# Kernel tuning notes

Hardware: AMD Instinct MI355X
Metric: run time of the kernel (lower is better)

The kernel has to match this reference:

```python
import jax, jax.numpy as jnp
import numpy as np

B, T, C, H, N = 2, 1024, 1024, 16, 64
D_DECAY, D_AAA, D_MV, D_GATE = 64, 64, 32, 128
LN_EPS = 64e-5  # GroupNorm eps used by RWKV7 (1e-5 * head_size_divisor**2)


def setup_inputs():
    key = jax.random.key(0)
    ks = jax.random.split(key, 32)
    rn = lambda k, shape, s=1.0: jax.random.normal(k, shape, jnp.float32) * s
    p = {}
    p['x'] = rn(ks[0], (B, T, C))
    p['v_first'] = rn(ks[1], (B, T, C))
    for i, nm in enumerate(['x_r', 'x_w', 'x_k', 'x_v', 'x_a', 'x_g']):
        p[nm] = jax.random.uniform(ks[2 + i], (1, 1, C), jnp.float32)
    p['w1'] = rn(ks[8], (C, D_DECAY), 0.02); p['w2'] = rn(ks[9], (D_DECAY, C), 0.02); p['w0'] = rn(ks[10], (C,), 0.5)
    p['a1'] = rn(ks[11], (C, D_AAA), 0.02); p['a2'] = rn(ks[12], (D_AAA, C), 0.02); p['a0'] = rn(ks[13], (C,), 0.1)
    p['v1'] = rn(ks[14], (C, D_MV), 0.02); p['v2'] = rn(ks[15], (D_MV, C), 0.02); p['v0'] = rn(ks[16], (C,), 0.1)
    p['g1'] = rn(ks[17], (C, D_GATE), 0.02); p['g2'] = rn(ks[18], (D_GATE, C), 0.02)
    p['k_k'] = jax.random.uniform(ks[19], (1, 1, C), jnp.float32)
    p['k_a'] = jax.random.uniform(ks[20], (1, 1, C), jnp.float32)
    p['r_k'] = rn(ks[21], (H, N), 0.1)
    s = C ** -0.5
    p['W_r'] = rn(ks[22], (C, C), s); p['W_k'] = rn(ks[23], (C, C), s)
    p['W_v'] = rn(ks[24], (C, C), s); p['W_o'] = rn(ks[25], (C, C), s)
    p['ln_w'] = jnp.ones((C,), jnp.float32); p['ln_b'] = jnp.zeros((C,), jnp.float32)
    return p


def _rwkv7_op(r, w, k, v, a, b):
    # r,w,k,v,a,b: (B,T,C). Per-head matrix-state recurrence:
    #   S_t = S_{t-1} * diag(decay_t) + (S_{t-1} @ a_t) b_t^T + v_t k_t^T ; out_t = S_t @ r_t
    f = lambda z: z.reshape(B, T, H, N).astype(jnp.float32).transpose(1, 0, 2, 3)  # (T,B,H,N)
    r_, k_, v_, a_, b_ = f(r), f(k), f(v), f(a), f(b)
    d_ = jnp.exp(-jnp.exp(f(w)))  # decay in (0,1)

    def step(S, inp):
        rt, dt, kt, vt, at, bt = inp  # each (B,H,N)
        sa = jnp.einsum('bhij,bhj->bhi', S, at)
        S = S * dt[:, :, None, :] + sa[..., None] * bt[:, :, None, :] + vt[..., None] * kt[:, :, None, :]
        return S, jnp.einsum('bhij,bhj->bhi', S, rt)

    S0 = jnp.zeros((B, H, N, N), jnp.float32)
    _, out = jax.lax.scan(step, S0, (r_, d_, k_, v_, a_, b_))
    return out.transpose(1, 0, 2, 3).reshape(B, T, C)


def _forward(x, v_first, x_r, x_w, x_k, x_v, x_a, x_g, w1, w2, w0, a1, a2, a0,
             v1, v2, v0, g1, g2, k_k, k_a, r_k, W_r, W_k, W_v, W_o, ln_w, ln_b):
    xx = jnp.pad(x, ((0, 0), (1, 0), (0, 0)))[:, :T] - x  # token shift
    xr = x + xx * x_r; xw = x + xx * x_w; xk = x + xx * x_k
    xv = x + xx * x_v; xa = x + xx * x_a; xg = x + xx * x_g
    r = xr @ W_r
    w = -jax.nn.softplus(-(jnp.tanh(xw @ w1) @ w2 + w0)) - 0.5
    k = xk @ W_k
    v = xv @ W_v
    v = v + (v_first - v) * jax.nn.sigmoid(xv @ v1 @ v2 + v0)  # layer_id > 0 branch
    a = jax.nn.sigmoid(xa @ a1 @ a2 + a0)
    g = jax.nn.sigmoid(xg @ g1) @ g2
    kk = (k * k_k).reshape(B, T, H, N)
    kk = (kk / jnp.maximum(jnp.linalg.norm(kk, axis=-1, keepdims=True), 1e-12)).reshape(B, T, C)
    k = k * (1.0 + (a - 1.0) * k_a)
    y = _rwkv7_op(r, w, k, v, -kk, kk * a)
    # GroupNorm(H groups over C) applied per token
    yh = y.reshape(B, T, H, N)
    mu = yh.mean(-1, keepdims=True)
    var = yh.var(-1, keepdims=True)
    y = ((yh - mu) / jnp.sqrt(var + LN_EPS)).reshape(B, T, C) * ln_w + ln_b
    rh = r.reshape(B, T, H, N); kh = k.reshape(B, T, H, N); vh = v.reshape(B, T, H, N)
    y = y + ((rh * kh * r_k).sum(-1, keepdims=True) * vh).reshape(B, T, C)
    return (y * g) @ W_o


def reference(x, v_first, x_r, x_w, x_k, x_v, x_a, x_g, w1, w2, w0, a1, a2, a0,
              v1, v2, v0, g1, g2, k_k, k_a, r_k, W_r, W_k, W_v, W_o, ln_w, ln_b):
    out = _forward(x, v_first, x_r, x_w, x_k, x_v, x_a, x_g, w1, w2, w0, a1, a2, a0,
                   v1, v2, v0, g1, g2, k_k, k_a, r_k, W_r, W_k, W_v, W_o, ln_w, ln_b)
    return (out, v_first)
```

## Files before the change

kernel.cpp:

```cpp
#include <hip/hip_runtime.h>
#include <hip/hip_bf16.h>
#include <cstdint>
#include <cstddef>

typedef __hip_bfloat16 bf16;
typedef __bf16 bf16x8 __attribute__((ext_vector_type(8)));
typedef float f32x4 __attribute__((ext_vector_type(4)));

#define BB 2
#define TT 1024
#define CC 1024
#define HH 16
#define PKS 448
#define PKB 1792
#define CH 8
#define NCH 4
#define STEPB 2048
#define CHB (CH * STEPB)
#define NC (TT / CH)

__device__ __forceinline__ bf16 f2b(float v){ return __float2bfloat16(v); }

__device__ __forceinline__ float hex_add(float x) {
    x += __int_as_float(__builtin_amdgcn_mov_dpp(__float_as_int(x), 0xB1, 0xF, 0xF, true));
    x += __int_as_float(__builtin_amdgcn_mov_dpp(__float_as_int(x), 0x4E, 0xF, 0xF, true));
    x += __int_as_float(__builtin_amdgcn_mov_dpp(__float_as_int(x), 0x141, 0xF, 0xF, true));
    x += __int_as_float(__builtin_amdgcn_mov_dpp(__float_as_int(x), 0x140, 0xF, 0xF, true));
    return x;
}

typedef __attribute__((address_space(3))) void as3_void;
typedef __attribute__((address_space(1))) const void as1_void;
__device__ __forceinline__ void gload_lds16(const void* g, void* l) {
    __builtin_amdgcn_global_load_lds((as1_void*)g, (as3_void*)l, 16, 0, 0);
}

struct TrDesc { const float* in; bf16* out; int R, S; };
struct TrArgs { TrDesc d[12]; };

__global__ __launch_bounds__(256) void transpose_batch(TrArgs args)
{
    TrDesc t = args.d[blockIdx.z];
    __shared__ float tile[32][33];
    int s0 = blockIdx.x * 32, r0 = blockIdx.y * 32;
    if (s0 >= t.S || r0 >= t.R) return;
    int tx = threadIdx.x & 31, ty = threadIdx.x >> 5;
#pragma unroll
    for (int i = 0; i < 4; i++) {
        int r = r0 + ty + i * 8, s = s0 + tx;
        if (r < t.R && s < t.S) tile[ty + i * 8][tx] = t.in[(size_t)r * t.S + s];
    }
    __syncthreads();
#pragma unroll
    for (int i = 0; i < 4; i++) {
        int s = s0 + ty + i * 8, r = r0 + tx;
        if (s < t.S && r < t.R) t.out[(size_t)s * t.R + r] = f2b(tile[tx][ty + i * 8]);
    }
}

__global__ __launch_bounds__(256) void mix_kernel(
    const float* __restrict__ x, const float* __restrict__ vfirst,
    const float* __restrict__ mr, const float* __restrict__ mw, const float* __restrict__ mk,
    const float* __restrict__ mv, const float* __restrict__ ma, const float* __restrict__ mg,
    bf16* __restrict__ xr, bf16* __restrict__ xw, bf16* __restrict__ xk,
    bf16* __restrict__ xv, bf16* __restrict__ xa, bf16* __restrict__ xg,
    float* __restrict__ vout)
{
    int row = blockIdx.x;
    int t = row & (TT - 1);
    size_t base = (size_t)row * CC;
    for (int c = threadIdx.x; c < CC; c += 256) {
        float xc = x[base + c];
        float xp = (t > 0) ? x[base - CC + c] : 0.f;
        float d = xp - xc;
        xr[base + c] = f2b(xc + d * mr[c]);
        xw[base + c] = f2b(xc + d * mw[c]);
        xk[base + c] = f2b(xc + d * mk[c]);
        xv[base + c] = f2b(xc + d * mv[c]);
        xa[base + c] = f2b(xc + d * ma[c]);
        xg[base + c] = f2b(xc + d * mg[c]);
        vout[base + c] = vfirst[base + c];
    }
}

template <class EmitF>
__device__ __forceinline__ void gemm_tile(const bf16* __restrict__ A, const bf16* __restrict__ BT,
                                          int K, int m0, int n0, EmitF emit)
{
    __shared__ __align__(16) bf16 Atile[128 * 32];
    __shared__ __align__(16) bf16 Btile[128 * 32];
    int tid = threadIdx.x;
    int w = tid >> 6, lane = tid & 63;
    int wr = w >> 1, wc = w & 1;
    int quad = lane >> 4, l16 = lane & 15;

    f32x4 zero = {0.f, 0.f, 0.f, 0.f};
    f32x4 acc[4][4];
#pragma unroll
    for (int i = 0; i < 4; i++)
#pragma unroll
        for (int j = 0; j < 4; j++) acc[i][j] = zero;

    int rr = lane >> 2;
    int cs = lane & 3;
    int ra0 = w * 32 + rr;
    int ra1 = ra0 + 16;
    int cg0 = cs ^ ((ra0 >> 1) & 3);
    int cg1 = cs ^ ((ra1 >> 1) & 3);

    for (int k0 = 0; k0 < K; k0 += 32) {
        uint4 av0 = *reinterpret_cast<const uint4*>(A  + (size_t)(m0 + ra0) * K + k0 + cg0 * 8);
        uint4 av1 = *reinterpret_cast<const uint4*>(A  + (size_t)(m0 + ra1) * K + k0 + cg1 * 8);
        uint4 bv0 = *reinterpret_cast<const uint4*>(BT + (size_t)(n0 + ra0) * K + k0 + cg0 * 8);
        uint4 bv1 = *reinterpret_cast<const uint4*>(BT + (size_t)(n0 + ra1) * K + k0 + cg1 * 8);
        __syncthreads();
        *reinterpret_cast<uint4*>(&Atile[ra0 * 32 + cs * 8]) = av0;
        *reinterpret_cast<uint4*>(&Atile[ra1 * 32 + cs * 8]) = av1;
        *reinterpret_cast<uint4*>(&Btile[ra0 * 32 + cs * 8]) = bv0;
        *reinterpret_cast<uint4*>(&Btile[ra1 * 32 + cs * 8]) = bv1;
        __syncthreads();

        bf16x8 af[4], bfr[4];
#pragma unroll
        for (int mi = 0; mi < 4; mi++) {
            int m = wr * 64 + mi * 16 + l16;
            int c2 = quad ^ ((m >> 1) & 3);
            af[mi] = *reinterpret_cast<const bf16x8*>(&Atile[m * 32 + c2 * 8]);
        }
#pragma unroll
        for (int ni = 0; ni < 4; ni++) {
            int n = wc * 64 + ni * 16 + l16;
            int c2 = quad ^ ((n >> 1) & 3);
            bfr[ni] = *reinterpret_cast<const bf16x8*>(&Btile[n * 32 + c2 * 8]);
        }
#pragma unroll
        for (int mi = 0; mi < 4; mi++)
#pragma unroll
            for (int ni = 0; ni < 4; ni++)
                acc[mi][ni] = __builtin_amdgcn_mfma_f32_16x16x32_bf16(af[mi], bfr[ni], acc[mi][ni], 0, 0, 0);
    }

#pragma unroll
    for (int mi = 0; mi < 4; mi++)
#pragma unroll
        for (int ni = 0; ni < 4; ni++)
#pragma unroll
            for (int rg = 0; rg < 4; rg++) {
                int m = m0 + wr * 64 + mi * 16 + quad * 4 + rg;
                int n = n0 + wc * 64 + ni * 16 + l16;
                emit(m, n, acc[mi][ni][rg]);
            }
}

struct B3Args { const bf16* A[3]; const bf16* BT[3]; float* out[3]; };
__global__ __launch_bounds__(256) void big3_kernel(B3Args args)
{
    int z = blockIdx.z;
    float* out = args.out[z];
    gemm_tile(args.A[z], args.BT[z], 1024, blockIdx.x * 128, blockIdx.y * 128,
              [&](int m, int n, float v) { out[(size_t)m * 1024 + n] = v; });
}

struct L1Desc { const bf16* A; const bf16* BT; bf16* outB; int N; int mode; };
struct L1Args { L1Desc d[4]; };
__global__ __launch_bounds__(256) void lora1_kernel(L1Args args)
{
    L1Desc dz = args.d[blockIdx.z];
    gemm_tile(dz.A, dz.BT, 1024, blockIdx.x * 128, 0,
              [&](int m, int n, float v) {
                  if (n < dz.N) {
                      float r = (dz.mode == 2) ? tanhf(v)
                              : (dz.mode == 3) ? 1.f / (1.f + expf(-v)) : v;
                      dz.outB[(size_t)m * dz.N + n] = f2b(r);
                  }
              });
}

struct L2Desc { const bf16* A; const bf16* BT; const float* bias; float* outF; int K; int mode; };
struct L2Args { L2Desc d[4]; const float* vraw; const float* vfirst; };
__global__ __launch_bounds__(256) void lora2_kernel(L2Args args)
{
    L2Desc dz = args.d[blockIdx.z];
    gemm_tile(dz.A, dz.BT, dz.K, blockIdx.x * 128, blockIdx.y * 128,
              [&](int m, int n, float v) {
                  size_t idx = (size_t)m * 1024 + n;
                  if (dz.mode == 4) {
                      float xx = v + dz.bias[n];
                      float ww = -log1pf(expf(-xx)) - 0.5f;
                      dz.outF[idx] = expf(-expf(ww));
                  } else if (dz.mode == 5) {
                      float xx = v + dz.bias[n];
                      dz.outF[idx] = 1.f / (1.f + expf(-xx));
                  } else if (dz.mode == 6) {
                      float gate = 1.f / (1.f + expf(-(v + dz.bias[n])));
                      float vr = args.vraw[idx];
                      dz.outF[idx] = vr + (args.vfirst[idx] - vr) * gate;
                  } else {
                      dz.outF[idx] = v;
                  }
              });
}

__global__ __launch_bounds__(256) void final_kernel(const bf16* __restrict__ A, const bf16* __restrict__ BT,
                                                    float* __restrict__ out)
{
    gemm_tile(A, BT, 1024, blockIdx.x * 128, blockIdx.y * 128,
              [&](int m, int n, float v) { out[(size_t)m * 1024 + n] = v; });
}

__global__ __launch_bounds__(256) void pack_kernel(
    float* __restrict__ k, const float* __restrict__ a, const float* __restrict__ r,
    const float* __restrict__ v, const float* __restrict__ dw,
    const float* __restrict__ kkw, const float* __restrict__ kaw,
    float* __restrict__ PK)
{
    int tid = threadIdx.x;
    int wave = tid >> 6, lane = tid & 63;
    int idx = blockIdx.x * 4 + wave;
    size_t off = (size_t)idx * 64 + lane;
    int c = (idx & 15) * 64 + lane;
    float kraw = k[off];
    float av = a[off];
    float kkv = kraw * kkw[c];
    float s = kkv * kkv;
#pragma unroll
    for (int m = 32; m; m >>= 1) s += __shfl_xor(s, m);
    float kkn = kkv / fmaxf(sqrtf(s), 1e-12f);
    float ks = kraw * (1.f + (av - 1.f) * kaw[c]);
    k[off] = ks;
    float bb = kkn * av;
    float rv = r[off];
    float dv = dw[off];
    float bt = bb * rv, ct = ks * rv;
#pragma unroll
    for (int m = 32; m; m >>= 1) { bt += __shfl_xor(bt, m); ct += __shfl_xor(ct, m); }
    int b = idx >> 14;
    int h = idx & 15;
    int t = (idx >> 4) & (TT - 1);
    size_t sidx = (size_t)(b * HH + h) * TT + t;
    float* pw = PK + sidx * PKS;
    pw[lane] = ks; pw[64 + lane] = kkn; pw[128 + lane] = bb; pw[192 + lane] = v[off];
    pw[256 + lane] = rv; pw[320 + lane] = dv;
    if (lane == 0) { pw[384] = bt; pw[385] = ct; }
}

struct SetR { f32x4 q, d, r, k, b; float vi; float2 bc; };

__device__ __forceinline__ void ds_load_set(SetR& s, const char* slot, int c16, int row)
{
    s.q  = *(const f32x4*)(slot + 256  + c16);
    s.d  = *(const f32x4*)(slot + 1280 + c16);
    s.r  = *(const f32x4*)(slot + 1024 + c16);
    s.k  = *(const f32x4*)(slot + 0    + c16);
    s.b  = *(const f32x4*)(slot + 512  + c16);
    s.vi = *(const float*)(slot + 768 + row * 4);
    s.bc = *(const float2*)(slot + 1536);
}

__device__ __forceinline__ float step4(const SetR& sd, f32x4& S)
{
    f32x4 Sd   = S * sd.d;
    f32x4 sacv = S * sd.q;
    f32x4 oacv = Sd * sd.r;
    float sar = (sacv[0] + sacv[1]) + (sacv[2] + sacv[3]);
    float od  = (oacv[0] + oacv[1]) + (oacv[2] + oacv[3]);
    sar = hex_add(sar);
    od  = hex_add(od);
    float sa = -sar;
    float o = fmaf(sd.vi, sd.bc.y, fmaf(sa, sd.bc.x, od));
    S = Sd + sa * sd.b + sd.vi * sd.k;
    return o;
}

__global__ __launch_bounds__(256, 1) void scan_kernel(
    const float* __restrict__ PK, float* __restrict__ ybuf)
{
    __shared__ __align__(16) char ring[NCH * CHB];
    const int tid = threadIdx.x;
    const int wid = tid >> 6, lane = tid & 63;
    const int xcd = blockIdx.x & 7, kk = blockIdx.x >> 3;
    const int bh = xcd * 4 + (kk >> 4);
    const int wq = kk & 15;
    const int b = bh >> 4, h = bh & 15;
    const int row = wq * 4 + (lane >> 4);
    const int c = lane & 15;
    const int c16 = c * 16;

    const char* base = (const char*)(PK + (size_t)bh * TT * PKS);
    const char* g1 = base + lane * 16;
    const char* g2 = g1 + 1024;

    auto stage_chunk = [&](int ci) {
        const char* p1 = g1 + (size_t)ci * CH * PKB;
        const char* p2 = g2 + (size_t)ci * CH * PKB;
        char* s = ring + (ci & (NCH - 1)) * CHB;
        for (int j = wid - 1; j < CH; j += 3) {
            gload_lds16(p1 + (size_t)j * PKB, s + j * STEPB);
            gload_lds16(p2 + (size_t)j * PKB, s + j * STEPB + 1024);
        }
    };

    if (wid > 0) {
        stage_chunk(0);
        stage_chunk(1);
        stage_chunk(2);
        asm volatile("s_waitcnt vmcnt(0)" ::: "memory");
    }
    __builtin_amdgcn_sched_barrier(0);
    __builtin_amdgcn_s_barrier();
    __builtin_amdgcn_sched_barrier(0);

    f32x4 S = {0.f, 0.f, 0.f, 0.f};
    SetR X, Y;
    if (wid == 0) ds_load_set(X, ring, c16, row);
    float* py = ybuf + (size_t)b * TT * CC + h * 64 + row;

    for (int i = 0; i < NC; i++) {
        if (wid == 0) {
            const char* sl  = ring + (i & (NCH - 1)) * CHB;
            const char* sln = ring + ((i + 1) & (NCH - 1)) * CHB;
            float o;
            ds_load_set(Y, sl + 1 * STEPB, c16, row); o = step4(X, S); if (c == 0) *py = o; py += CC;
            ds_load_set(X, sl + 2 * STEPB, c16, row); o = step4(Y, S); if (c == 0) *py = o; py += CC;
            ds_load_set(Y, sl + 3 * STEPB, c16, row); o = step4(X, S); if (c == 0) *py = o; py += CC;
            ds_load_set(X, sl + 4 * STEPB, c16, row); o = step4(Y, S); if (c == 0) *py = o; py += CC;
            ds_load_set(Y, sl + 5 * STEPB, c16, row); o = step4(X, S); if (c == 0) *py = o; py += CC;
            ds_load_set(X, sl + 6 * STEPB, c16, row); o = step4(Y, S); if (c == 0) *py = o; py += CC;
            ds_load_set(Y, sl + 7 * STEPB, c16, row); o = step4(X, S); if (c == 0) *py = o; py += CC;
            ds_load_set(X, sln,            c16, row); o = step4(Y, S); if (c == 0) *py = o; py += CC;
        } else {
            if (i + 3 < NC) {
                stage_chunk(i + 3);
                if (wid == 3) asm volatile("s_waitcnt vmcnt(4)" ::: "memory");
                else          asm volatile("s_waitcnt vmcnt(6)" ::: "memory");
            } else {
                asm volatile("s_waitcnt vmcnt(0)" ::: "memory");
            }
        }
        __builtin_amdgcn_sched_barrier(0);
        __builtin_amdgcn_s_barrier();
        __builtin_amdgcn_sched_barrier(0);
    }
}

__global__ __launch_bounds__(256) void gn_kernel(
    const float* __restrict__ y, const float* __restrict__ r, const float* __restrict__ k,
    const float* __restrict__ v, const float* __restrict__ g,
    const float* __restrict__ lnw, const float* __restrict__ lnb,
    const float* __restrict__ rk, bf16* __restrict__ z)
{
    int tid = threadIdx.x;
    int idx = blockIdx.x * 4 + (tid >> 6);
    int lane = tid & 63;
    size_t off = (size_t)idx * 64 + lane;
    int c = (idx & 15) * 64 + lane;
    float yv = y[off];
    float rv = r[off], kv = k[off], vv = v[off];
    float s1 = yv, s2 = yv * yv, s3 = rv * kv * rk[c];
#pragma unroll
    for (int m = 32; m; m >>= 1) {
        s1 += __shfl_xor(s1, m);
        s2 += __shfl_xor(s2, m);
        s3 += __shfl_xor(s3, m);
    }
    float mu = s1 * (1.f / 64.f);
    float var = fmaxf(s2 * (1.f / 64.f) - mu * mu, 0.f);
    float yn = (yv - mu) * rsqrtf(var + 64e-5f) * lnw[c] + lnb[c];
    float out = (yn + s3 * vv) * g[off];
    z[off] = f2b(out);
}

extern "C" void kernel_launch(void* const* d_in, const int* in_sizes, int n_in,
                              void* d_out, int out_size, void* d_ws, size_t ws_size,
                              hipStream_t stream)
{
    const float* x       = (const float*)d_in[0];
    const float* v_first = (const float*)d_in[1];
    const float* x_r = (const float*)d_in[2];
    const float* x_w = (const float*)d_in[3];
    const float* x_k = (const float*)d_in[4];
    const float* x_v = (const float*)d_in[5];
    const float* x_a = (const float*)d_in[6];
    const float* x_g = (const float*)d_in[7];
    const float* w1 = (const float*)d_in[8];
    const float* w2 = (const float*)d_in[9];
    const float* w0 = (const float*)d_in[10];
    const float* a1 = (const float*)d_in[11];
    const float* a2 = (const float*)d_in[12];
    const float* a0 = (const float*)d_in[13];
    const float* v1 = (const float*)d_in[14];
    const float* v2 = (const float*)d_in[15];
    const float* v0 = (const float*)d_in[16];
    const float* g1 = (const float*)d_in[17];
    const float* g2 = (const float*)d_in[18];
    const float* k_k = (const float*)d_in[19];
    const float* k_a = (const float*)d_in[20];
    const float* r_k = (const float*)d_in[21];
    const float* W_r = (const float*)d_in[22];
    const float* W_k = (const float*)d_in[23];
    const float* W_v = (const float*)d_in[24];
    const float* W_o = (const float*)d_in[25];
    const float* ln_w = (const float*)d_in[26];
    const float* ln_b = (const float*)d_in[27];

    const size_t BTC = (size_t)BB * TT * CC;
    const int M = BB * TT;

    char* ws = (char*)d_ws;
    size_t off = 0;
    auto alloc = [&](size_t bytes) -> char* {
        char* p = ws + off;
        off += (bytes + 255) & ~(size_t)255;
        return p;
    };

    bf16* xr = (bf16*)alloc(BTC * 2);
    bf16* xw = (bf16*)alloc(BTC * 2);
    bf16* xk = (bf16*)alloc(BTC * 2);
    bf16* xv = (bf16*)alloc(BTC * 2);
    bf16* xa = (bf16*)alloc(BTC * 2);
    bf16* xg = (bf16*)alloc(BTC * 2);
    bf16* WrT = (bf16*)alloc(1024 * 1024 * 2);
    bf16* WkT = (bf16*)alloc(1024 * 1024 * 2);
    bf16* WvT = (bf16*)alloc(1024 * 1024 * 2);
    bf16* w1T = (bf16*)alloc(128 * 1024 * 2);
    bf16* a1T = (bf16*)alloc(128 * 1024 * 2);
    bf16* v1T = (bf16*)alloc(128 * 1024 * 2);
    bf16* g1T = (bf16*)alloc(128 * 1024 * 2);
    bf16* w2T = (bf16*)alloc(1024 * 64 * 2);
    bf16* a2T = (bf16*)alloc(1024 * 64 * 2);
    bf16* v2T = (bf16*)alloc(1024 * 32 * 2);
    bf16* g2T = (bf16*)alloc(1024 * 128 * 2);
    bf16* h_w = (bf16*)alloc((size_t)M * 64 * 2);
    bf16* h_a = (bf16*)alloc((size_t)M * 64 * 2);
    bf16* h_v = (bf16*)alloc((size_t)M * 32 * 2);
    bf16* h_g = (bf16*)alloc((size_t)M * 128 * 2);

    float* PK = (float*)ws;
    size_t pk_end = (size_t)BB * HH * TT * PKS * 4;
    if (off < pk_end) off = pk_end;
    off = (off + 255) & ~(size_t)255;

    bf16* WoT = (bf16*)alloc(1024 * 1024 * 2);
    float* rbuf = (float*)alloc(BTC * 4);
    float* kbuf = (float*)alloc(BTC * 4);
    float* vraw = (float*)alloc(BTC * 4);
    float* vbuf = (float*)alloc(BTC * 4);
    float* dbuf = (float*)alloc(BTC * 4);
    float* abuf = (float*)alloc(BTC * 4);
    float* gbuf = (float*)alloc(BTC * 4);

    float* ybuf = vraw;
    bf16*  zbuf = (bf16*)dbuf;

    (void)in_sizes; (void)n_in; (void)out_size; (void)ws_size;

    TrArgs ta;
    ta.d[0]  = {W_r, WrT, 1024, 1024};
    ta.d[1]  = {W_k, WkT, 1024, 1024};
    ta.d[2]  = {W_v, WvT, 1024, 1024};
    ta.d[3]  = {W_o, WoT, 1024, 1024};
    ta.d[4]  = {w1, w1T, 1024, 64};
    ta.d[5]  = {a1, a1T, 1024, 64};
    ta.d[6]  = {v1, v1T, 1024, 32};
    ta.d[7]  = {g1, g1T, 1024, 128};
    ta.d[8]  = {w2, w2T, 64, 1024};
    ta.d[9]  = {a2, a2T, 64, 1024};
    ta.d[10] = {v2, v2T, 32, 1024};
    ta.d[11] = {g2, g2T, 128, 1024};
    transpose_batch<<<dim3(32, 32, 12), 256, 0, stream>>>(ta);

    float* vout = (float*)d_out + BTC;
    mix_kernel<<<BB * TT, 256, 0, stream>>>(x, v_first, x_r, x_w, x_k, x_v, x_a, x_g,
                                            xr, xw, xk, xv, xa, xg, vout);

    B3Args b3;
    b3.A[0] = xr; b3.A[1] = xk; b3.A[2] = xv;
    b3.BT[0] = WrT; b3.BT[1] = WkT; b3.BT[2] = WvT;
    b3.out[0] = rbuf; b3.out[1] = kbuf; b3.out[2] = vraw;
    big3_kernel<<<dim3(16, 8, 3), 256, 0, stream>>>(b3);

    L1Args l1;
    l1.d[0] = {xw, w1T, h_w, 64, 2};
    l1.d[1] = {xa, a1T, h_a, 64, 0};
    l1.d[2] = {xv, v1T, h_v, 32, 0};
    l1.d[3] = {xg, g1T, h_g, 128, 3};
    lora1_kernel<<<dim3(16, 1, 4), 256, 0, stream>>>(l1);

    L2Args l2;
    l2.d[0] = {h_w, w2T, w0, dbuf, 64, 4};
    l2.d[1] = {h_a, a2T, a0, abuf, 64, 5};
    l2.d[2] = {h_v, v2T, v0, vbuf, 32, 6};
    l2.d[3] = {h_g, g2T, nullptr, gbuf, 128, 0};
    l2.vraw = vraw; l2.vfirst = v_first;
    lora2_kernel<<<dim3(16, 8, 4), 256, 0, stream>>>(l2);

    pack_kernel<<<BB * TT * HH / 4, 256, 0, stream>>>(kbuf, abuf, rbuf, vbuf, dbuf, k_k, k_a, PK);

    scan_kernel<<<BB * HH * 16, 256, 0, stream>>>(PK, ybuf);

    gn_kernel<<<BB * TT * HH / 4, 256, 0, stream>>>(ybuf, rbuf, kbuf, vbuf, gbuf, ln_w, ln_b, r_k, zbuf);

    final_kernel<<<dim3(16, 8), 256, 0, stream>>>(zbuf, WoT, (float*)d_out);
}
```

Measured before the change: 426.3 us.

## Merge prep launches, fuse projection and LoRA-down GEMMs, use direct global-to-LDS loads

The weight-transpose and token-mix kernels become one launch, with the mix work placed in an extra z-slice. The three big projections and the four LoRA-down GEMMs now share a single launch, and LoRA blocks with y>0 exit early. The GEMM tile loader now uses global_load_lds so data goes straight from global memory into LDS without passing through registers. The aim is to cut launch overhead and tail gaps and to lower register pressure during staging. The LDS layout from direct loads must match the swizzled reads the old explicit stores produced, which is a correctness risk.

```diff
diff --git a/kernel.cpp b/kernel.cpp
--- a/kernel.cpp
+++ b/kernel.cpp
@@ -36,50 +36,53 @@
 }
 
 struct TrDesc { const float* in; bf16* out; int R, S; };
-struct TrArgs { TrDesc d[12]; };
-
-__global__ __launch_bounds__(256) void transpose_batch(TrArgs args)
-{
-    TrDesc t = args.d[blockIdx.z];
-    __shared__ float tile[32][33];
-    int s0 = blockIdx.x * 32, r0 = blockIdx.y * 32;
-    if (s0 >= t.S || r0 >= t.R) return;
-    int tx = threadIdx.x & 31, ty = threadIdx.x >> 5;
-#pragma unroll
-    for (int i = 0; i < 4; i++) {
-        int r = r0 + ty + i * 8, s = s0 + tx;
-        if (r < t.R && s < t.S) tile[ty + i * 8][tx] = t.in[(size_t)r * t.S + s];
-    }
-    __syncthreads();
-#pragma unroll
-    for (int i = 0; i < 4; i++) {
-        int s = s0 + ty + i * 8, r = r0 + tx;
-        if (s < t.S && r < t.R) t.out[(size_t)s * t.R + r] = f2b(tile[tx][ty + i * 8]);
-    }
-}
-
-__global__ __launch_bounds__(256) void mix_kernel(
-    const float* __restrict__ x, const float* __restrict__ vfirst,
-    const float* __restrict__ mr, const float* __restrict__ mw, const float* __restrict__ mk,
-    const float* __restrict__ mv, const float* __restrict__ ma, const float* __restrict__ mg,
-    bf16* __restrict__ xr, bf16* __restrict__ xw, bf16* __restrict__ xk,
-    bf16* __restrict__ xv, bf16* __restrict__ xa, bf16* __restrict__ xg,
-    float* __restrict__ vout)
-{
-    int row = blockIdx.x;
-    int t = row & (TT - 1);
-    size_t base = (size_t)row * CC;
-    for (int c = threadIdx.x; c < CC; c += 256) {
-        float xc = x[base + c];
-        float xp = (t > 0) ? x[base - CC + c] : 0.f;
-        float d = xp - xc;
-        xr[base + c] = f2b(xc + d * mr[c]);
-        xw[base + c] = f2b(xc + d * mw[c]);
-        xk[base + c] = f2b(xc + d * mk[c]);
-        xv[base + c] = f2b(xc + d * mv[c]);
-        xa[base + c] = f2b(xc + d * ma[c]);
-        xg[base + c] = f2b(xc + d * mg[c]);
-        vout[base + c] = vfirst[base + c];
+struct PrepArgs {
+    TrDesc d[12];
+    const float* x; const float* vfirst;
+    const float *mr, *mw, *mk, *mv, *ma, *mg;
+    bf16 *xr, *xw, *xk, *xv, *xa, *xg;
+    float* vout;
+};
+
+__global__ __launch_bounds__(256) void prep_kernel(PrepArgs args)
+{
+    if (blockIdx.z < 12) {
+        TrDesc t = args.d[blockIdx.z];
+        __shared__ float tile[32][33];
+        int s0 = blockIdx.x * 32, r0 = blockIdx.y * 32;
+        if (s0 >= t.S || r0 >= t.R) return;
+        int tx = threadIdx.x & 31, ty = threadIdx.x >> 5;
+#pragma unroll
+        for (int i = 0; i < 4; i++) {
+            int r = r0 + ty + i * 8, s = s0 + tx;
+            if (r < t.R && s < t.S) tile[ty + i * 8][tx] = t.in[(size_t)r * t.S + s];
+        }
+        __syncthreads();
+#pragma unroll
+        for (int i = 0; i < 4; i++) {
+            int s = s0 + ty + i * 8, r = r0 + tx;
+            if (s < t.S && r < t.R) t.out[(size_t)s * t.R + r] = f2b(tile[tx][ty + i * 8]);
+        }
+        return;
+    }
+    int bid = blockIdx.y * 32 + blockIdx.x;
+#pragma unroll
+    for (int rr = 0; rr < 2; rr++) {
+        int row = bid * 2 + rr;
+        int t = row & (TT - 1);
+        size_t base = (size_t)row * CC;
+        for (int c = threadIdx.x; c < CC; c += 256) {
+            float xc = args.x[base + c];
+            float xp = (t > 0) ? args.x[base - CC + c] : 0.f;
+            float d = xp - xc;
+            args.xr[base + c] = f2b(xc + d * args.mr[c]);
+            args.xw[base + c] = f2b(xc + d * args.mw[c]);
+            args.xk[base + c] = f2b(xc + d * args.mk[c]);
+            args.xv[base + c] = f2b(xc + d * args.mv[c]);
+            args.xa[base + c] = f2b(xc + d * args.ma[c]);
+            args.xg[base + c] = f2b(xc + d * args.mg[c]);
+            args.vout[base + c] = args.vfirst[base + c];
+        }
     }
 }
 
@@ -108,16 +111,15 @@
     int cg0 = cs ^ ((ra0 >> 1) & 3);
     int cg1 = cs ^ ((ra1 >> 1) & 3);
 
+    bf16* atb = Atile + w * 1024;
+    bf16* btb = Btile + w * 1024;
+
     for (int k0 = 0; k0 < K; k0 += 32) {
-        uint4 av0 = *reinterpret_cast<const uint4*>(A  + (size_t)(m0 + ra0) * K + k0 + cg0 * 8);
-        uint4 av1 = *reinterpret_cast<const uint4*>(A  + (size_t)(m0 + ra1) * K + k0 + cg1 * 8);
-        uint4 bv0 = *reinterpret_cast<const uint4*>(BT + (size_t)(n0 + ra0) * K + k0 + cg0 * 8);
-        uint4 bv1 = *reinterpret_cast<const uint4*>(BT + (size_t)(n0 + ra1) * K + k0 + cg1 * 8);
         __syncthreads();
-        *reinterpret_cast<uint4*>(&Atile[ra0 * 32 + cs * 8]) = av0;
-        *reinterpret_cast<uint4*>(&Atile[ra1 * 32 + cs * 8]) = av1;
-        *reinterpret_cast<uint4*>(&Btile[ra0 * 32 + cs * 8]) = bv0;
-        *reinterpret_cast<uint4*>(&Btile[ra1 * 32 + cs * 8]) = bv1;
+        gload_lds16(A  + (size_t)(m0 + ra0) * K + k0 + cg0 * 8, atb);
+        gload_lds16(A  + (size_t)(m0 + ra1) * K + k0 + cg1 * 8, atb + 512);
+        gload_lds16(BT + (size_t)(n0 + ra0) * K + k0 + cg0 * 8, btb);
+        gload_lds16(BT + (size_t)(n0 + ra1) * K + k0 + cg1 * 8, btb + 512);
         __syncthreads();
 
         bf16x8 af[4], bfr[4];
@@ -152,20 +154,20 @@
             }
 }
 
-struct B3Args { const bf16* A[3]; const bf16* BT[3]; float* out[3]; };
-__global__ __launch_bounds__(256) void big3_kernel(B3Args args)
+struct L1Desc { const bf16* A; const bf16* BT; bf16* outB; int N; int mode; };
+struct ProjArgs { const bf16* A[3]; const bf16* BT[3]; float* out[3]; L1Desc d[4]; };
+
+__global__ __launch_bounds__(256) void proj_kernel(ProjArgs args)
 {
     int z = blockIdx.z;
-    float* out = args.out[z];
-    gemm_tile(args.A[z], args.BT[z], 1024, blockIdx.x * 128, blockIdx.y * 128,
-              [&](int m, int n, float v) { out[(size_t)m * 1024 + n] = v; });
-}
-
-struct L1Desc { const bf16* A; const bf16* BT; bf16* outB; int N; int mode; };
-struct L1Args { L1Desc d[4]; };
-__global__ __launch_bounds__(256) void lora1_kernel(L1Args args)
-{
-    L1Desc dz = args.d[blockIdx.z];
+    if (z < 3) {
+        float* out = args.out[z];
+        gemm_tile(args.A[z], args.BT[z], 1024, blockIdx.x * 128, blockIdx.y * 128,
+                  [&](int m, int n, float v) { out[(size_t)m * 1024 + n] = v; });
+        return;
+    }
+    if (blockIdx.y) return;
+    L1Desc dz = args.d[z - 3];
     gemm_tile(dz.A, dz.BT, 1024, blockIdx.x * 128, 0,
               [&](int m, int n, float v) {
                   if (n < dz.N) {
@@ -455,37 +457,34 @@
 
     (void)in_sizes; (void)n_in; (void)out_size; (void)ws_size;
 
-    TrArgs ta;
-    ta.d[0]  = {W_r, WrT, 1024, 1024};
-    ta.d[1]  = {W_k, WkT, 1024, 1024};
-    ta.d[2]  = {W_v, WvT, 1024, 1024};
-    ta.d[3]  = {W_o, WoT, 1024, 1024};
-    ta.d[4]  = {w1, w1T, 1024, 64};
-    ta.d[5]  = {a1, a1T, 1024, 64};
-    ta.d[6]  = {v1, v1T, 1024, 32};
-    ta.d[7]  = {g1, g1T, 1024, 128};
-    ta.d[8]  = {w2, w2T, 64, 1024};
-    ta.d[9]  = {a2, a2T, 64, 1024};
-    ta.d[10] = {v2, v2T, 32, 1024};
-    ta.d[11] = {g2, g2T, 128, 1024};
-    transpose_batch<<<dim3(32, 32, 12), 256, 0, stream>>>(ta);
-
-    float* vout = (float*)d_out + BTC;
-    mix_kernel<<<BB * TT, 256, 0, stream>>>(x, v_first, x_r, x_w, x_k, x_v, x_a, x_g,
-                                            xr, xw, xk, xv, xa, xg, vout);
-
-    B3Args b3;
-    b3.A[0] = xr; b3.A[1] = xk; b3.A[2] = xv;
-    b3.BT[0] = WrT; b3.BT[1] = WkT; b3.BT[2] = WvT;
-    b3.out[0] = rbuf; b3.out[1] = kbuf; b3.out[2] = vraw;
-    big3_kernel<<<dim3(16, 8, 3), 256, 0, stream>>>(b3);
-
-    L1Args l1;
-    l1.d[0] = {xw, w1T, h_w, 64, 2};
-    l1.d[1] = {xa, a1T, h_a, 64, 0};
-    l1.d[2] = {xv, v1T, h_v, 32, 0};
-    l1.d[3] = {xg, g1T, h_g, 128, 3};
-    lora1_kernel<<<dim3(16, 1, 4), 256, 0, stream>>>(l1);
+    PrepArgs pa;
+    pa.d[0]  = {W_r, WrT, 1024, 1024};
+    pa.d[1]  = {W_k, WkT, 1024, 1024};
+    pa.d[2]  = {W_v, WvT, 1024, 1024};
+    pa.d[3]  = {W_o, WoT, 1024, 1024};
+    pa.d[4]  = {w1, w1T, 1024, 64};
+    pa.d[5]  = {a1, a1T, 1024, 64};
+    pa.d[6]  = {v1, v1T, 1024, 32};
+    pa.d[7]  = {g1, g1T, 1024, 128};
+    pa.d[8]  = {w2, w2T, 64, 1024};
+    pa.d[9]  = {a2, a2T, 64, 1024};
+    pa.d[10] = {v2, v2T, 32, 1024};
+    pa.d[11] = {g2, g2T, 128, 1024};
+    pa.x = x; pa.vfirst = v_first;
+    pa.mr = x_r; pa.mw = x_w; pa.mk = x_k; pa.mv = x_v; pa.ma = x_a; pa.mg = x_g;
+    pa.xr = xr; pa.xw = xw; pa.xk = xk; pa.xv = xv; pa.xa = xa; pa.xg = xg;
+    pa.vout = (float*)d_out + BTC;
+    prep_kernel<<<dim3(32, 32, 13), 256, 0, stream>>>(pa);
+
+    ProjArgs pj;
+    pj.A[0] = xr; pj.A[1] = xk; pj.A[2] = xv;
+    pj.BT[0] = WrT; pj.BT[1] = WkT; pj.BT[2] = WvT;
+    pj.out[0] = rbuf; pj.out[1] = kbuf; pj.out[2] = vraw;
+    pj.d[0] = {xw, w1T, h_w, 64, 2};
+    pj.d[1] = {xa, a1T, h_a, 64, 0};
+    pj.d[2] = {xv, v1T, h_v, 32, 0};
+    pj.d[3] = {xg, g1T, h_g, 128, 3};
+    proj_kernel<<<dim3(16, 8, 7), 256, 0, stream>>>(pj);
 
     L2Args l2;
     l2.d[0] = {h_w, w2T, w0, dbuf, 64, 4};
```

New measurement: 423.6 us. Within noise of the previous version (-0.6%).
